# Kernel tuning notes

Measured on AMD Instinct MI355X. Metric: run time of the kernel, lower is better.

## Reference

```python
import jax, jax.numpy as jnp
import numpy as np


def setup_inputs() -> dict:
    key = jax.random.key(0)
    ks = jax.random.split(key, 5)
    B, T, D, U = 32, 2048, 512, 512
    scale = 1.0 / np.sqrt(D)
    return {
        "full": jax.random.normal(ks[0], (B, T, D), jnp.float32),
        "last": jax.random.normal(ks[1], (B, D), jnp.float32),
        "W1": jax.random.normal(ks[2], (D, U), jnp.float32) * scale,
        "b1": jnp.zeros((U,), jnp.float32),
        "W2": jax.random.normal(ks[3], (D, U), jnp.float32) * scale,
        "b2": jnp.zeros((U,), jnp.float32),
        "V": jax.random.normal(ks[4], (U, 1), jnp.float32) * (1.0 / np.sqrt(U)),
        "bV": jnp.zeros((1,), jnp.float32),
    }


def reference(full, last, W1, b1, W2, b2, V, bV):
    # full: [B,T,D], last: [B,D]
    h1 = jnp.einsum("btd,du->btu", full, W1) + b1          # [B,T,U]
    h2 = last @ W2 + b2                                      # [B,U]
    score = jnp.tanh(h1 + h2[:, None, :]) @ V + bV           # [B,T,1]
    attn = jax.nn.softmax(score, axis=1)                     # [B,T,1]
    context = jnp.sum(attn * full, axis=1)                   # [B,D]
    return context
```

## Files before the change

### kernel.cpp

```cpp
#include <hip/hip_runtime.h>
#include <math.h>


#define BB 32
#define TT 2048
#define DD 512
#define UU 512
#define BKK 32
#define KSTEPS 16

typedef short bf16x8 __attribute__((ext_vector_type(8)));
typedef float f32x4  __attribute__((ext_vector_type(4)));

static __device__ __forceinline__ short f2bf(float f) {
    unsigned x = __float_as_uint(f);
    return (short)((x + 0x7fffu + ((x >> 16) & 1u)) >> 16);
}

static __device__ __forceinline__ float fast_tanh(float x) {
    float e = __expf(2.f * x);
    return 1.f - 2.f * __builtin_amdgcn_rcpf(e + 1.f);
}

__global__ __launch_bounds__(256) void prep_kernel(const float* __restrict__ W1,
                                                   short* __restrict__ W1T,
                                                   const float* __restrict__ last,
                                                   const float* __restrict__ W2,
                                                   const float* __restrict__ b1,
                                                   const float* __restrict__ b2,
                                                   float* __restrict__ h2) {
    __shared__ float tile[32][33];
    __shared__ float ls[DD];
    __shared__ float part[256];
    const int bid = blockIdx.x;
    const int tid = threadIdx.x;
    if (bid < 256) {
        const int tr = (bid >> 4) << 5;
        const int tc = (bid & 15) << 5;
#pragma unroll
        for (int p = 0; p < 4; ++p) {
            const int r = p * 8 + (tid >> 5), c = tid & 31;
            tile[r][c] = W1[(size_t)(tr + r) * UU + tc + c];
        }
        __syncthreads();
#pragma unroll
        for (int p = 0; p < 4; ++p) {
            const int r = p * 8 + (tid >> 5), c = tid & 31;
            W1T[(size_t)(tc + r) * DD + tr + c] = f2bf(tile[c][r]);
        }
    } else {
        const int b2i = bid - 256;
        const int b  = b2i >> 2;
        const int u0 = (b2i & 3) << 7;
        for (int i = tid; i < DD; i += 256) ls[i] = last[b * DD + i];
        __syncthreads();
        const int uu = tid & 127;
        const int dh = tid >> 7;
        float acc = 0.f;
#pragma unroll 8
        for (int d = dh * 256; d < dh * 256 + 256; ++d)
            acc += ls[d] * W2[d * UU + u0 + uu];
        part[tid] = acc;
        __syncthreads();
        if (tid < 128) {
            const int u = u0 + tid;
            h2[b * UU + u] = part[tid] + part[tid + 128] + b1[u] + b2[u];
        }
    }
}

__global__ __launch_bounds__(512) void score_kernel(const float* __restrict__ full,
                                                    const short* __restrict__ W1T,
                                                    const float* __restrict__ h2,
                                                    const float* __restrict__ V,
                                                    float* __restrict__ ctx,
                                                    float* __restrict__ m_arr,
                                                    float* __restrict__ l_arr) {
    __shared__ __align__(16) float a32[2][128 * BKK];
    __shared__ __align__(16) short blds[2][512 * BKK];
    __shared__ float red64[8][64];
    __shared__ float esc[128];
    __shared__ float sred[8];
    __shared__ __align__(16) float red4[4][128][4];

    const int bid = blockIdx.x;
    const int b    = bid >> 4;
    const int t0   = (bid & 15) << 7;
    const int tid  = threadIdx.x;
    const int w    = tid >> 6;
    const int lane = tid & 63;
    const int quad = lane >> 4;
    const int col  = lane & 15;
    const int wm   = w >> 2;
    const int wn   = w & 3;

    f32x4 acc[4][8];
#pragma unroll
    for (int i = 0; i < 4; ++i)
#pragma unroll
        for (int j = 0; j < 8; ++j) acc[i][j] = (f32x4){0.f, 0.f, 0.f, 0.f};

    const size_t fullbase = (size_t)(b * TT + t0) * DD;

#define STAGE(bufidx, koidx) do {                                                     \
        _Pragma("unroll")                                                             \
        for (int i = 0; i < 2; ++i) {                                                 \
            const int sb = w * 128 + i * 64;                                          \
            const int s  = sb + lane;                                                 \
            const int r  = s >> 3;                                                    \
            const int cc = (s & 7) ^ (r & 7);                                         \
            const float* g = &full[fullbase + (size_t)r * DD + (koidx) * BKK + cc * 4]; \
            __builtin_amdgcn_global_load_lds(                                         \
                (const __attribute__((address_space(1))) void*)g,                     \
                (__attribute__((address_space(3))) void*)&a32[bufidx][sb * 4], 16, 0, 0); \
        }                                                                             \
        _Pragma("unroll")                                                             \
        for (int i = 0; i < 4; ++i) {                                                 \
            const int sb = w * 256 + i * 64;                                          \
            const int s  = sb + lane;                                                 \
            const int u  = s >> 2;                                                    \
            const int kc = (s & 3) ^ ((u >> 1) & 3);                                  \
            const short* g = &W1T[(size_t)u * DD + (koidx) * BKK + kc * 8];           \
            __builtin_amdgcn_global_load_lds(                                         \
                (const __attribute__((address_space(1))) void*)g,                     \
                (__attribute__((address_space(3))) void*)&blds[bufidx][sb * 8], 16, 0, 0); \
        }                                                                             \
    } while (0)

    STAGE(0, 0);
    __syncthreads();

    int cur = 0;
    for (int ko = 0; ko < KSTEPS; ++ko) {
        if (ko < KSTEPS - 1) STAGE(cur ^ 1, ko + 1);

        bf16x8 af[4];
#pragma unroll
        for (int mt = 0; mt < 4; ++mt) {
            const int r  = wm * 64 + mt * 16 + col;
            const int c0 = quad * 2;
            const f32x4 lo = *(const f32x4*)&a32[cur][(r * 8 + (c0 ^ (r & 7))) * 4];
            const f32x4 hi = *(const f32x4*)&a32[cur][(r * 8 + ((c0 + 1) ^ (r & 7))) * 4];
            af[mt] = (bf16x8){f2bf(lo.x), f2bf(lo.y), f2bf(lo.z), f2bf(lo.w),
                              f2bf(hi.x), f2bf(hi.y), f2bf(hi.z), f2bf(hi.w)};
        }
#pragma unroll
        for (int nt = 0; nt < 8; ++nt) {
            const int u = wn * 128 + nt * 16 + col;
            const bf16x8 bf = *(const bf16x8*)&blds[cur][(u * 4 + (quad ^ ((u >> 1) & 3))) * 8];
#pragma unroll
            for (int mt = 0; mt < 4; ++mt)
                acc[mt][nt] = __builtin_amdgcn_mfma_f32_16x16x32_bf16(af[mt], bf, acc[mt][nt], 0, 0, 0);
        }
        __syncthreads();
        cur ^= 1;
    }
#undef STAGE

    float srow[16];
#pragma unroll
    for (int i = 0; i < 16; ++i) srow[i] = 0.f;
#pragma unroll
    for (int nt = 0; nt < 8; ++nt) {
        const int u = wn * 128 + nt * 16 + col;
        const float hv = h2[b * UU + u];
        const float vv = V[u];
#pragma unroll
        for (int mt = 0; mt < 4; ++mt)
#pragma unroll
            for (int r = 0; r < 4; ++r)
                srow[mt * 4 + r] += fast_tanh(acc[mt][nt][r] + hv) * vv;
    }
#pragma unroll
    for (int off = 1; off < 16; off <<= 1) {
#pragma unroll
        for (int i = 0; i < 16; ++i) srow[i] += __shfl_xor(srow[i], off, 64);
    }
    if (col == 0) {
#pragma unroll
        for (int mt = 0; mt < 4; ++mt)
#pragma unroll
            for (int r = 0; r < 4; ++r)
                red64[w][mt * 16 + quad * 4 + r] = srow[mt * 4 + r];
    }
    __syncthreads();

    float sv = 0.f;
    if (tid < 128) {
        const int wmX = tid >> 6, rr = tid & 63;
        sv = red64[wmX * 4 + 0][rr] + red64[wmX * 4 + 1][rr] +
             red64[wmX * 4 + 2][rr] + red64[wmX * 4 + 3][rr];
        float mv = sv;
#pragma unroll
        for (int off = 1; off < 64; off <<= 1) mv = fmaxf(mv, __shfl_xor(mv, off, 64));
        if (lane == 0) sred[w] = mv;
    }
    __syncthreads();
    const float M = fmaxf(sred[0], sred[1]);
    if (tid < 128) {
        float e = __expf(sv - M);
        esc[tid] = e;
#pragma unroll
        for (int off = 1; off < 64; off <<= 1) e += __shfl_xor(e, off, 64);
        if (lane == 0) sred[4 + w] = e;
    }
    __syncthreads();
    if (tid == 0) { m_arr[bid] = M; l_arr[bid] = sred[4] + sred[5]; }

    const int c  = tid & 127;
    const int tp = tid >> 7;
    float ax = 0.f, ay = 0.f, az = 0.f, aw = 0.f;
#pragma unroll 4
    for (int i = 0; i < 32; ++i) {
        const int t = i * 4 + tp;
        const float4 v = *(const float4*)&full[fullbase + (size_t)t * DD + c * 4];
        const float e = esc[t];
        ax += e * v.x; ay += e * v.y; az += e * v.z; aw += e * v.w;
    }
    *(float4*)&red4[tp][c][0] = make_float4(ax, ay, az, aw);
    __syncthreads();
    if (tp == 0) {
        const float4 p0 = *(const float4*)&red4[0][c][0];
        const float4 p1 = *(const float4*)&red4[1][c][0];
        const float4 p2 = *(const float4*)&red4[2][c][0];
        const float4 p3 = *(const float4*)&red4[3][c][0];
        float4 s = make_float4(p0.x + p1.x + p2.x + p3.x,
                               p0.y + p1.y + p2.y + p3.y,
                               p0.z + p1.z + p2.z + p3.z,
                               p0.w + p1.w + p2.w + p3.w);
        *(float4*)&ctx[(size_t)bid * DD + c * 4] = s;
    }
}

__global__ __launch_bounds__(256) void combine_kernel(const float* __restrict__ ctx,
                                                      const float* __restrict__ m_arr,
                                                      const float* __restrict__ l_arr,
                                                      float* __restrict__ out) {
    const int b = blockIdx.x;
    const int tid = threadIdx.x;
    __shared__ float wgt[16];
    __shared__ float linv;
    if (tid == 0) {
        float M = -1e30f;
#pragma unroll
        for (int i = 0; i < 16; ++i) M = fmaxf(M, m_arr[b * 16 + i]);
        float l = 0.f;
#pragma unroll
        for (int i = 0; i < 16; ++i) {
            wgt[i] = __expf(m_arr[b * 16 + i] - M);
            l += wgt[i] * l_arr[b * 16 + i];
        }
        linv = 1.f / l;
    }
    __syncthreads();
    float s0 = 0.f, s1 = 0.f;
#pragma unroll
    for (int i = 0; i < 16; ++i) {
        const float wi = wgt[i];
        const float* cp = &ctx[(size_t)(b * 16 + i) * DD + tid * 2];
        s0 += wi * cp[0];
        s1 += wi * cp[1];
    }
    out[b * DD + tid * 2]     = s0 * linv;
    out[b * DD + tid * 2 + 1] = s1 * linv;
}

extern "C" void kernel_launch(void* const* d_in, const int* in_sizes, int n_in,
                              void* d_out, int out_size, void* d_ws, size_t ws_size,
                              hipStream_t stream) {
    const float* full = (const float*)d_in[0];
    const float* last = (const float*)d_in[1];
    const float* W1   = (const float*)d_in[2];
    const float* b1   = (const float*)d_in[3];
    const float* W2   = (const float*)d_in[4];
    const float* b2   = (const float*)d_in[5];
    const float* V    = (const float*)d_in[6];

    float* out   = (float*)d_out;
    float* h2    = (float*)d_ws;
    float* m_arr = h2 + (size_t)BB * UU;
    float* l_arr = m_arr + 512;
    float* ctx   = l_arr + 512;
    short* W1T   = (short*)(ctx + (size_t)BB * 16 * DD);

    prep_kernel<<<384, 256, 0, stream>>>(W1, W1T, last, W2, b1, b2, h2);
    score_kernel<<<BB * 16, 512, 0, stream>>>(full, W1T, h2, V, ctx, m_arr, l_arr);
    combine_kernel<<<BB, 256, 0, stream>>>(ctx, m_arr, l_arr, out);
}
```

Before: 264.8 us.

## Prefetch two K-steps ahead with register-staged LDS reads and fine-grained waits

```diff
diff --git a/kernel.cpp b/kernel.cpp
--- a/kernel.cpp
+++ b/kernel.cpp
@@ -128,31 +128,49 @@
     } while (0)
 
     STAGE(0, 0);
-    __syncthreads();
+    STAGE(1, 1);
+    asm volatile("s_waitcnt vmcnt(6)" ::: "memory");
+    __builtin_amdgcn_s_barrier();
 
     int cur = 0;
     for (int ko = 0; ko < KSTEPS; ++ko) {
-        if (ko < KSTEPS - 1) STAGE(cur ^ 1, ko + 1);
-
-        bf16x8 af[4];
+        f32x4 alo[4], ahi[4];
+        bf16x8 bfr[8];
 #pragma unroll
         for (int mt = 0; mt < 4; ++mt) {
             const int r  = wm * 64 + mt * 16 + col;
             const int c0 = quad * 2;
-            const f32x4 lo = *(const f32x4*)&a32[cur][(r * 8 + (c0 ^ (r & 7))) * 4];
-            const f32x4 hi = *(const f32x4*)&a32[cur][(r * 8 + ((c0 + 1) ^ (r & 7))) * 4];
-            af[mt] = (bf16x8){f2bf(lo.x), f2bf(lo.y), f2bf(lo.z), f2bf(lo.w),
-                              f2bf(hi.x), f2bf(hi.y), f2bf(hi.z), f2bf(hi.w)};
+            alo[mt] = *(const f32x4*)&a32[cur][(r * 8 + (c0 ^ (r & 7))) * 4];
+            ahi[mt] = *(const f32x4*)&a32[cur][(r * 8 + ((c0 + 1) ^ (r & 7))) * 4];
         }
 #pragma unroll
         for (int nt = 0; nt < 8; ++nt) {
             const int u = wn * 128 + nt * 16 + col;
-            const bf16x8 bf = *(const bf16x8*)&blds[cur][(u * 4 + (quad ^ ((u >> 1) & 3))) * 8];
+            bfr[nt] = *(const bf16x8*)&blds[cur][(u * 4 + (quad ^ ((u >> 1) & 3))) * 8];
+        }
+        asm volatile("s_waitcnt lgkmcnt(0)" ::: "memory");
+        __builtin_amdgcn_sched_barrier(0);
+        __builtin_amdgcn_s_barrier();
+
+        if (ko + 2 < KSTEPS) STAGE(cur, ko + 2);
+
+        bf16x8 af[4];
+#pragma unroll
+        for (int mt = 0; mt < 4; ++mt)
+            af[mt] = (bf16x8){f2bf(alo[mt].x), f2bf(alo[mt].y), f2bf(alo[mt].z), f2bf(alo[mt].w),
+                              f2bf(ahi[mt].x), f2bf(ahi[mt].y), f2bf(ahi[mt].z), f2bf(ahi[mt].w)};
+#pragma unroll
+        for (int nt = 0; nt < 8; ++nt)
 #pragma unroll
             for (int mt = 0; mt < 4; ++mt)
-                acc[mt][nt] = __builtin_amdgcn_mfma_f32_16x16x32_bf16(af[mt], bf, acc[mt][nt], 0, 0, 0);
-        }
-        __syncthreads();
+                acc[mt][nt] = __builtin_amdgcn_mfma_f32_16x16x32_bf16(af[mt], bfr[nt], acc[mt][nt], 0, 0, 0);
+
+        if (ko < KSTEPS - 2) {
+            asm volatile("s_waitcnt vmcnt(6)" ::: "memory");
+        } else if (ko == KSTEPS - 2) {
+            asm volatile("s_waitcnt vmcnt(0)" ::: "memory");
+        }
+        if (ko < KSTEPS - 1) __builtin_amdgcn_s_barrier();
         cur ^= 1;
     }
 #undef STAGE
```

New measurement: 259.9 us. No clear change (-1.9%).
